# Kernel optimization log

Measured on AMD Instinct MI355X. Metric: run time of the kernel, lower is better.

The kernel has to match this reference:

```python
import jax, jax.numpy as jnp
import numpy as np

B, N, D = 512, 120, 64
NB = 8  # n_freq_bands
S_CLIP, DELTA_CLIP = 10.0, 5.0


def zc_rms(x, g, eps=1e-8):
    # zero-centred RMS norm
    x0 = x - x0_mean(x)
    return x0 * jax.lax.rsqrt(jnp.mean(x0 * x0, axis=-1, keepdims=True) + eps) * g


def x0_mean(x):
    return jnp.mean(x, axis=-1, keepdims=True)


def l2norm(x, eps=1e-8):
    return x * jax.lax.rsqrt(jnp.sum(x * x, axis=-1, keepdims=True) + eps)


def setup_inputs() -> dict:
    key = jax.random.key(0)
    ks = jax.random.split(key, 12)
    s = 1.0 / np.sqrt(D)
    return {
        "x": jax.random.normal(ks[0], (B, N, D), dtype=jnp.float32),
        "g_norm": jnp.ones((D,), jnp.float32),
        "Wq": jax.random.normal(ks[1], (D, D), jnp.float32) * s,
        "Wk": jax.random.normal(ks[2], (D, D), jnp.float32) * s,
        "Wv": jax.random.normal(ks[3], (D, D), jnp.float32) * s,
        "bv": jnp.zeros((D,), jnp.float32),
        "Wo": jax.random.normal(ks[4], (D, D), jnp.float32) * s,
        "bo": jnp.zeros((D,), jnp.float32),
        "g_post": jnp.ones((D,), jnp.float32),
        "W1": jax.random.normal(ks[5], (NB, 16), jnp.float32) * (1.0 / np.sqrt(NB)),
        "b1": jnp.zeros((16,), jnp.float32),
        "W2": jax.random.normal(ks[6], (16, 1), jnp.float32) * 0.25,
        "b2": jnp.full((1,), 0.5, jnp.float32),  # bias init 0.5 as in torch
    }


def _gamma(h, W1, b1, W2, b2):
    # FFT over embedding dim, band-averaged energies -> gate in [0.5, 0.99]
    fft = jnp.abs(jnp.fft.rfft(jax.lax.stop_gradient(h), axis=-1))  # (B,N,n_f)
    n_f = fft.shape[-1]
    bs = max(1, n_f // NB)
    bands = [fft[..., i * bs:min(i * bs + bs, n_f)].mean(-1) for i in range(NB)]
    energy = jnp.stack(bands, axis=-1)  # (B,N,NB)
    energy = energy / jnp.clip(jnp.sum(energy, axis=-1, keepdims=True), 1e-8)
    hdn = jax.nn.silu(energy @ W1 + b1)
    raw = jax.nn.sigmoid(hdn @ W2 + b2)  # (B,N,1)
    return 0.5 + 0.49 * raw


def reference(x, g_norm, Wq, Wk, Wv, bv, Wo, bo, g_post, W1, b1, W2, b2):
    h = zc_rms(x, g_norm)
    q = l2norm(h @ Wq)
    k = l2norm(h @ Wk)
    v = h @ Wv + bv
    gamma = _gamma(h, W1, b1, W2, b2)  # (B,N,1)

    # time-major for scan
    qT = jnp.moveaxis(q, 1, 0)      # (N,B,D)
    kT = jnp.moveaxis(k, 1, 0)
    vT = jnp.moveaxis(v, 1, 0)
    gT = jnp.moveaxis(gamma, 1, 0)  # (N,B,1)

    S0 = jnp.zeros((x.shape[0], D, D), x.dtype)

    def step(S, inp):
        q_t, k_t, v_t, g_t = inp
        pred = jnp.einsum('bde,be->bd', S, k_t)
        delta = jnp.clip(v_t - pred, -DELTA_CLIP, DELTA_CLIP)
        S = g_t[..., None] * S + delta[:, :, None] * k_t[:, None, :]
        S = jnp.clip(S, -S_CLIP, S_CLIP)
        o_t = jnp.einsum('bde,be->bd', S, q_t)
        return S, o_t

    _, outT = jax.lax.scan(step, S0, (qT, kT, vT, gT))
    out = jnp.moveaxis(outT, 0, 1)  # (B,N,D)
    out = zc_rms(out, g_post) @ Wo + bo  # dropout is identity at inference
    return x + out
```

## Files before the change

kernel.cpp:

```cpp
#include <hip/hip_runtime.h>
#include <math.h>

#define B_ 512
#define N_ 120

typedef __attribute__((ext_vector_type(8))) _Float16 f16x8;
typedef __attribute__((ext_vector_type(4))) _Float16 f16x4;
typedef __attribute__((ext_vector_type(2))) _Float16 f16x2;
typedef __attribute__((ext_vector_type(4))) float f32x4;
typedef __attribute__((ext_vector_type(2))) float f32x2;
typedef __attribute__((ext_vector_type(4))) int i32x4;

#define DPP_XOR1 0xB1
#define DPP_XOR2 0x4E
#define DPP_HMIR 0x141
#define DPP_MIR  0x140
template<int CTRL>
__device__ __forceinline__ float dpp_add(float v) {
    int x = __builtin_amdgcn_mov_dpp(__float_as_int(v), CTRL, 0xF, 0xF, true);
    return v + __int_as_float(x);
}

__device__ __forceinline__ float mix_lo(float a, int b, float c) {
    float d;
    asm("v_fma_mix_f32 %0, %1, %2, %3 op_sel:[0,0,0] op_sel_hi:[0,1,0]"
        : "=v"(d) : "v"(a), "v"(b), "v"(c));
    return d;
}
__device__ __forceinline__ float mix_hi(float a, int b, float c) {
    float d;
    asm("v_fma_mix_f32 %0, %1, %2, %3 op_sel:[0,1,0] op_sel_hi:[0,1,0]"
        : "=v"(d) : "v"(a), "v"(b), "v"(c));
    return d;
}
__device__ __forceinline__ f32x2 pk_mul2(f32x2 a, f32x2 b) {
    f32x2 d;
    asm("v_pk_mul_f32 %0, %1, %2" : "=v"(d) : "v"(a), "v"(b));
    return d;
}
__device__ __forceinline__ int pkrtz_i32(float a, float b) {
    auto sp = __builtin_amdgcn_cvt_pkrtz(a, b);
    return *(int*)&sp;
}

#define OFF_WQ 0
#define OFF_WK 4096
#define OFF_WV 8192
#define OFF_T  12288
#define OFF_XF 16384
#define OFF_QS 0
#define OFF_KS 7680
#define OFF_VS 15360
#define OFF_OF 23040
#define OFF_WO 31232
#define LDS_F16 35328

__device__ __forceinline__ void mm4(f16x8 a0, f16x8 a1, const _Float16* wmat,
                                    int lane, f32x4* acc) {
    const f16x8* wv = (const f16x8*)wmat;
    #pragma unroll
    for (int nt = 0; nt < 4; ++nt) {
        f32x4 z = {0.f, 0.f, 0.f, 0.f};
        z = __builtin_amdgcn_mfma_f32_16x16x32_f16(a0, wv[nt * 128 + lane], z, 0, 0, 0);
        z = __builtin_amdgcn_mfma_f32_16x16x32_f16(a1, wv[nt * 128 + 64 + lane], z, 0, 0, 0);
        acc[nt] = z;
    }
}

__global__ __launch_bounds__(512, 4) void fused_kdn(
    const float* __restrict__ x, const float* __restrict__ g_norm,
    const float* __restrict__ Wq, const float* __restrict__ Wk,
    const float* __restrict__ Wv, const float* __restrict__ bv,
    const float* __restrict__ Wo, const float* __restrict__ bo,
    const float* __restrict__ g_post,
    const float* __restrict__ W1, const float* __restrict__ b1,
    const float* __restrict__ W2, const float* __restrict__ b2,
    float* out)
{
    __shared__ __align__(16) _Float16 L[LDS_F16];
    __shared__ __align__(16) float g_s[N_];
    __shared__ float bv_s[64], bo_s[64];
    __shared__ float sW1[128], sb1[16], sW2[16], sb2_s[1];

    int tid = threadIdx.x, wave = tid >> 6, lane = tid & 63;
    int b = blockIdx.x;

    if (tid < 128) sW1[tid] = W1[tid];
    if (tid >= 128 && tid < 144) sb1[tid - 128] = b1[tid - 128];
    if (tid >= 144 && tid < 160) sW2[tid - 144] = W2[tid - 144];
    if (tid == 160) sb2_s[0] = b2[0];
    if (tid >= 192 && tid < 256) bv_s[tid - 192] = bv[tid - 192];
    if (tid >= 256 && tid < 320) bo_s[tid - 256] = bo[tid - 256];
    if (tid < 128) {
        f16x8 z = {0, 0, 0, 0, 0, 0, 0, 0};
        *(f16x8*)&L[OFF_XF + 7168 + tid * 8] = z;
        *(f16x8*)&L[OFF_OF + 7168 + tid * 8] = z;
    }
    int sn = tid & 63, sk0 = (tid >> 6) * 8;
    int widx = (sn >> 4) * 1024 + (sk0 >> 5) * 512 + ((((sk0 >> 3) & 3) << 4) + (sn & 15)) * 8;
    {
        const float* Ws[4] = { Wq, Wk, Wv, Wo };
        const int woff[4] = { OFF_WQ, OFF_WK, OFF_WV, OFF_WO };
        #pragma unroll
        for (int m = 0; m < 4; ++m) {
            f16x8 pv;
            #pragma unroll
            for (int j = 0; j < 8; ++j) pv[j] = (_Float16)Ws[m][(sk0 + j) * 64 + sn];
            *(f16x8*)&L[woff[m] + widx] = pv;
        }
        f16x8 pv;
        int nn = sn & 31;
        #pragma unroll
        for (int j = 0; j < 8; ++j) {
            int kk = ((sk0 + j) * nn) & 63;
            float a = (float)kk * (6.283185307179586f / 64.0f);
            float s, c; __sincosf(a, &s, &c);
            pv[j] = (_Float16)((sn < 32) ? c : s);
        }
        *(f16x8*)&L[OFF_T + widx] = pv;
    }
    __syncthreads();

    const float* xb = x + (size_t)b * N_ * 64;
    float* ob_g = out + (size_t)b * N_ * 64;

    {
        float gn = g_norm[lane];
        int hbase = (lane >> 5) * 512 + ((lane >> 3) & 3) * 128 + (lane & 7);
        #pragma unroll 5
        for (int c = 0; c < 15; ++c) {
            int row = wave * 15 + c;
            float xv = xb[row * 64 + lane];
            float sx = xv, sxx = xv * xv;
            sx = dpp_add<DPP_XOR1>(sx); sxx = dpp_add<DPP_XOR1>(sxx);
            sx = dpp_add<DPP_XOR2>(sx); sxx = dpp_add<DPP_XOR2>(sxx);
            sx = dpp_add<DPP_HMIR>(sx); sxx = dpp_add<DPP_HMIR>(sxx);
            sx = dpp_add<DPP_MIR >(sx); sxx = dpp_add<DPP_MIR >(sxx);
            sx += __shfl_xor(sx, 16);   sxx += __shfl_xor(sxx, 16);
            sx += __shfl_xor(sx, 32);   sxx += __shfl_xor(sxx, 32);
            float mean = sx * 0.015625f;
            float var  = sxx * 0.015625f - mean * mean;
            float h = (xv - mean) * rsqrtf(var + 1e-8f) * gn;
            float hp = __shfl_xor(h, 1);
            if (!(lane & 1)) {
                f16x2 pk2 = { (_Float16)h, (_Float16)hp };
                *(f16x2*)&L[OFF_XF + (row >> 4) * 1024 + (row & 15) * 8 + hbase] = pk2;
            }
        }
    }
    __syncthreads();

    int grp = lane >> 4, li = lane & 15;
    int rbase = wave * 16 + grp * 4;
    {
        const f16x8* hfv = (const f16x8*)(L + OFF_XF);
        f16x8 a0 = hfv[wave * 128 + lane];
        f16x8 a1 = hfv[wave * 128 + 64 + lane];
        f32x4 accT[4];

        mm4(a0, a1, L + OFF_T, lane, accT);
        {
            int gb2 = lane & 48;
            #pragma unroll
            for (int reg = 0; reg < 4; ++reg) {
                float re1 = accT[0][reg], re2 = accT[1][reg];
                float im1 = accT[2][reg], im2 = accT[3][reg];
                float m1 = sqrtf(fmaf(re1, re1, im1 * im1));
                float m2 = sqrtf(fmaf(re2, re2, im2 * im2));
                m1 = dpp_add<DPP_XOR1>(m1); m2 = dpp_add<DPP_XOR1>(m2);
                m1 = dpp_add<DPP_XOR2>(m1); m2 = dpp_add<DPP_XOR2>(m2);
                float e1 = m1 * 0.25f, e2 = m2 * 0.25f;
                float tot = e1 + e2;
                tot = dpp_add<DPP_HMIR>(tot);
                tot = dpp_add<DPP_MIR >(tot);
                float rinv = 1.0f / fmaxf(tot, 1e-8f);
                float en1 = e1 * rinv, en2 = e2 * rinv;
                float hs = sb1[li];
                #pragma unroll
                for (int i = 0; i < 4; ++i)
                    hs = fmaf(__shfl(en1, gb2 + (i << 2)), sW1[i * 16 + li], hs);
                #pragma unroll
                for (int i = 0; i < 4; ++i)
                    hs = fmaf(__shfl(en2, gb2 + (i << 2)), sW1[(i + 4) * 16 + li], hs);
                float act = hs / (1.0f + __expf(-hs));
                float p = act * sW2[li];
                p = dpp_add<DPP_XOR1>(p);
                p = dpp_add<DPP_XOR2>(p);
                p = dpp_add<DPP_HMIR>(p);
                p = dpp_add<DPP_MIR >(p);
                float raw = 1.0f / (1.0f + __expf(-(p + sb2_s[0])));
                int row = rbase + reg;
                if (li == 0 && row < N_) g_s[row] = fmaf(0.49f, raw, 0.5f);
            }
        }

        f32x4 accq[4], acck[4], accv[4];
        mm4(a0, a1, L + OFF_WQ, lane, accq);
        mm4(a0, a1, L + OFF_WK, lane, acck);
        mm4(a0, a1, L + OFF_WV, lane, accv);

        {
            f32x4 sq = accq[0]*accq[0] + accq[1]*accq[1] + accq[2]*accq[2] + accq[3]*accq[3];
            f32x4 sk = acck[0]*acck[0] + acck[1]*acck[1] + acck[2]*acck[2] + acck[3]*acck[3];
            #pragma unroll
            for (int reg = 0; reg < 4; ++reg) {
                float qs = sq[reg], ks = sk[reg];
                qs = dpp_add<DPP_XOR1>(qs); ks = dpp_add<DPP_XOR1>(ks);
                qs = dpp_add<DPP_XOR2>(qs); ks = dpp_add<DPP_XOR2>(ks);
                qs = dpp_add<DPP_HMIR>(qs); ks = dpp_add<DPP_HMIR>(ks);
                qs = dpp_add<DPP_MIR >(qs); ks = dpp_add<DPP_MIR >(ks);
                float rq = rsqrtf(qs + 1e-8f), rk = rsqrtf(ks + 1e-8f);
                #pragma unroll
                for (int nt = 0; nt < 4; ++nt) { accq[nt][reg] *= rq; acck[nt][reg] *= rk; }
            }
            #pragma unroll
            for (int nt = 0; nt < 4; ++nt) {
                float bvn = bv_s[nt * 16 + li];
                #pragma unroll
                for (int reg = 0; reg < 4; ++reg) accv[nt][reg] += bvn;
            }
        }
        __syncthreads();

        #pragma unroll
        for (int reg = 0; reg < 4; ++reg) {
            int row = rbase + reg;
            if (row < N_) {
                int base = row * 64 + li;
                #pragma unroll
                for (int nt = 0; nt < 4; ++nt) {
                    L[OFF_QS + base + nt * 16] = (_Float16)accq[nt][reg];
                    L[OFF_KS + base + nt * 16] = (_Float16)acck[nt][reg];
                    L[OFF_VS + base + nt * 16] = (_Float16)accv[nt][reg];
                }
            }
        }
    }
    __syncthreads();

    if (wave < 4) {
        int col = lane & 15;
        int kg  = lane >> 4;
        int c0  = kg * 8;
        int d0  = wave * 16 + kg * 4;
        int dpart = (d0 >> 5) * 512 + ((d0 >> 3) & 3) * 128 + (d0 & 7);
        const _Float16* ksp = L + OFF_KS;
        const _Float16* qsp = L + OFF_QS;
        const _Float16* vsp = L + OFF_VS;
        const _Float16* bbase = (col == 0) ? (qsp + c0) : (ksp + 64 + c0);
        const _Float16* vown = vsp + d0 + (col & 3);
        int srcli = (col & 3) ? (col & 3) : 4;
        int bp_addr = (((col >> 2) << 4) + srcli) << 2;

        f32x2 S2[8];
        #pragma unroll
        for (int j = 0; j < 8; ++j) { S2[j].x = 0.f; S2[j].y = 0.f; }
        f32x4 ppC = {0.f, 0.f, 0.f, 0.f};
        const float fone = 1.0f, fzero = 0.0f;
        float4 gq = *(const float4*)&g_s[0];

#define UPD2(j, KW, DST)                                                       \
        {                                                                      \
            f32x2 t2 = pk_mul2(gt2, S2[j]);                                    \
            float sa = mix_lo(delta, KW, t2.x);                                \
            float sb = mix_hi(delta, KW, t2.y);                                \
            sa = __builtin_amdgcn_fmed3f(sa, -10.f, 10.f);                     \
            sb = __builtin_amdgcn_fmed3f(sb, -10.f, 10.f);                     \
            S2[j].x = sa; S2[j].y = sb;                                        \
            DST = pkrtz_i32(sa, sb);                                           \
        }

#define SCAN_IT(T, GT)                                                         \
        {                                                                      \
            int   vv  = (int)*(const unsigned short*)&vown[(T) * 64];          \
            f16x8 ku0 = *(const f16x8*)&ksp[(T) * 64 + c0];                    \
            f16x8 ku1 = *(const f16x8*)&ksp[(T) * 64 + c0 + 32];               \
            f16x8 b0  = *(const f16x8*)&bbase[(T) * 64];                       \
            f16x8 b1  = *(const f16x8*)&bbase[(T) * 64 + 32];                  \
            float gt = (GT);                                                   \
            f32x2 gt2; gt2.x = gt; gt2.y = gt;                                 \
            float pA = (col & 1) ? ppC[1] : ppC[0];                            \
            float pB = (col & 1) ? ppC[3] : ppC[2];                            \
            float pown = (col & 2) ? pB : pA;                                  \
            float vf = mix_lo(fone, vv, fzero);                                \
            float dloc = __builtin_amdgcn_fmed3f(vf - pown, -5.f, 5.f);        \
            float delta = __int_as_float(                                      \
                __builtin_amdgcn_ds_bpermute(bp_addr, __float_as_int(dloc)));  \
            i32x4 k0i = *(i32x4*)&ku0;                                         \
            i32x4 k1i = *(i32x4*)&ku1;                                         \
            i32x4 a0i, a1i;                                                    \
            UPD2(0, k0i[0], a0i[0]) UPD2(1, k0i[1], a0i[1])                    \
            UPD2(2, k0i[2], a0i[2]) UPD2(3, k0i[3], a0i[3])                    \
            UPD2(4, k1i[0], a1i[0]) UPD2(5, k1i[1], a1i[1])                    \
            UPD2(6, k1i[2], a1i[2]) UPD2(7, k1i[3], a1i[3])                    \
            f16x8 a0s = *(f16x8*)&a0i;                                         \
            f16x8 a1s = *(f16x8*)&a1i;                                         \
            f32x4 C = {0.f, 0.f, 0.f, 0.f};                                    \
            C = __builtin_amdgcn_mfma_f32_16x16x32_f16(a0s, b0, C, 0, 0, 0);   \
            C = __builtin_amdgcn_mfma_f32_16x16x32_f16(a1s, b1, C, 0, 0, 0);   \
            if (col == 0) {                                                    \
                f16x4 o4 = { (_Float16)C[0], (_Float16)C[1],                   \
                             (_Float16)C[2], (_Float16)C[3] };                 \
                int oidx = OFF_OF + (((T) >> 4) * 1024) + (((T) & 15) * 8) + dpart; \
                *(f16x4*)&L[oidx] = o4;                                        \
            }                                                                  \
            ppC = C;                                                           \
        }

        for (int t4 = 0; t4 < N_; t4 += 4) {
            float4 gq_n = (t4 + 4 < N_) ? *(const float4*)&g_s[t4 + 4] : gq;
            SCAN_IT(t4 + 0, gq.x)
            SCAN_IT(t4 + 1, gq.y)
            SCAN_IT(t4 + 2, gq.z)
            SCAN_IT(t4 + 3, gq.w)
            gq = gq_n;
        }
#undef SCAN_IT
#undef UPD2
    }
    __syncthreads();

    {
        float gp = g_post[lane];
        int hbase = (lane >> 5) * 512 + ((lane >> 3) & 3) * 128 + (lane & 7);
        #pragma unroll 5
        for (int c = 0; c < 15; ++c) {
            int row = wave * 15 + c;
            int ridx = OFF_OF + (row >> 4) * 1024 + (row & 15) * 8;
            float ov = (float)L[ridx + hbase];
            float sx = ov, sxx = ov * ov;
            sx = dpp_add<DPP_XOR1>(sx); sxx = dpp_add<DPP_XOR1>(sxx);
            sx = dpp_add<DPP_XOR2>(sx); sxx = dpp_add<DPP_XOR2>(sxx);
            sx = dpp_add<DPP_HMIR>(sx); sxx = dpp_add<DPP_HMIR>(sxx);
            sx = dpp_add<DPP_MIR >(sx); sxx = dpp_add<DPP_MIR >(sxx);
            sx += __shfl_xor(sx, 16);   sxx += __shfl_xor(sxx, 16);
            sx += __shfl_xor(sx, 32);   sxx += __shfl_xor(sxx, 32);
            float mean = sx * 0.015625f;
            float var  = sxx * 0.015625f - mean * mean;
            float hn = (ov - mean) * rsqrtf(var + 1e-8f) * gp;
            float hp = __shfl_xor(hn, 1);
            if (!(lane & 1)) {
                f16x2 pk2 = { (_Float16)hn, (_Float16)hp };
                *(f16x2*)&L[ridx + hbase] = pk2;
            }
        }
    }
    __syncthreads();

    {
        const f16x8* hfv = (const f16x8*)(L + OFF_OF);
        f16x8 a0 = hfv[wave * 128 + lane];
        f16x8 a1 = hfv[wave * 128 + 64 + lane];
        f32x4 acc[4];
        mm4(a0, a1, L + OFF_WO, lane, acc);
        #pragma unroll
        for (int reg = 0; reg < 4; ++reg) {
            int row = rbase + reg;
            if (row < N_) {
                #pragma unroll
                for (int nt = 0; nt < 4; ++nt) {
                    int idx = row * 64 + nt * 16 + li;
                    ob_g[idx] = acc[nt][reg] + bo_s[nt * 16 + li] + xb[idx];
                }
            }
        }
    }
}

extern "C" void kernel_launch(void* const* d_in, const int* in_sizes, int n_in,
                              void* d_out, int out_size, void* d_ws, size_t ws_size,
                              hipStream_t stream)
{
    const float* x      = (const float*)d_in[0];
    const float* g_norm = (const float*)d_in[1];
    const float* Wq     = (const float*)d_in[2];
    const float* Wk     = (const float*)d_in[3];
    const float* Wv     = (const float*)d_in[4];
    const float* bv     = (const float*)d_in[5];
    const float* Wo     = (const float*)d_in[6];
    const float* bo     = (const float*)d_in[7];
    const float* g_post = (const float*)d_in[8];
    const float* W1     = (const float*)d_in[9];
    const float* b1     = (const float*)d_in[10];
    const float* W2     = (const float*)d_in[11];
    const float* b2     = (const float*)d_in[12];
    float* out = (float*)d_out;

    fused_kdn<<<B_, 512, 0, stream>>>(x, g_norm, Wq, Wk, Wv, bv, Wo, bo, g_post,
                                      W1, b1, W2, b2, out);
}
```

Measured before the change: 146.8 us.

## Restructure scan MFMA so state is B operand and delta computed without bpermute

The recurrence inner step now uses the updated state as the MFMA B operand, with q and the next k as A operands, in two separate MFMA pairs. The output and the next step's prediction land directly in the lane that owns each row. The v term is folded in as the accumulator init (-v), which removes the ds_bpermute cross-lane shuffle and the per-lane select of the previous C from the serial dependency chain. In exchange it issues four MFMAs per step instead of two, and the final iteration reads k and v one row past N, which may touch out-of-range shared memory.

```diff
diff --git a/kernel.cpp b/kernel.cpp
--- a/kernel.cpp
+++ b/kernel.cpp
@@ -242,21 +242,26 @@
         int col = lane & 15;
         int kg  = lane >> 4;
         int c0  = kg * 8;
-        int d0  = wave * 16 + kg * 4;
-        int dpart = (d0 >> 5) * 512 + ((d0 >> 3) & 3) * 128 + (d0 & 7);
-        const _Float16* ksp = L + OFF_KS;
-        const _Float16* qsp = L + OFF_QS;
-        const _Float16* vsp = L + OFF_VS;
-        const _Float16* bbase = (col == 0) ? (qsp + c0) : (ksp + 64 + c0);
-        const _Float16* vown = vsp + d0 + (col & 3);
-        int srcli = (col & 3) ? (col & 3) : 4;
-        int bp_addr = (((col >> 2) << 4) + srcli) << 2;
+        int dd  = wave * 16 + col;
+        int dpart = (dd >> 5) * 512 + ((dd >> 3) & 3) * 128 + (dd & 7);
+        const _Float16* ksp  = L + OFF_KS;
+        const _Float16* qsp  = L + OFF_QS;
+        const _Float16* vown = L + OFF_VS + dd;
 
         f32x2 S2[8];
         #pragma unroll
         for (int j = 0; j < 8; ++j) { S2[j].x = 0.f; S2[j].y = 0.f; }
-        f32x4 ppC = {0.f, 0.f, 0.f, 0.f};
-        const float fone = 1.0f, fzero = 0.0f;
+        const float fzero = 0.0f, fnegone = -1.0f;
+
+        f16x8 ku0 = *(const f16x8*)&ksp[c0];
+        f16x8 ku1 = *(const f16x8*)&ksp[c0 + 32];
+        float delta;
+        {
+            int vv0 = (int)*(const unsigned short*)&vown[0];
+            float mv = mix_lo(fnegone, vv0, fzero);
+            float dneg = __builtin_amdgcn_fmed3f(mv, -5.f, 5.f);
+            delta = __int_as_float(__float_as_int(dneg) ^ 0x80000000);
+        }
         float4 gq = *(const float4*)&g_s[0];
 
 #define UPD2(j, KW, DST)                                                       \
@@ -272,20 +277,13 @@
 
 #define SCAN_IT(T, GT)                                                         \
         {                                                                      \
-            int   vv  = (int)*(const unsigned short*)&vown[(T) * 64];          \
-            f16x8 ku0 = *(const f16x8*)&ksp[(T) * 64 + c0];                    \
-            f16x8 ku1 = *(const f16x8*)&ksp[(T) * 64 + c0 + 32];               \
-            f16x8 b0  = *(const f16x8*)&bbase[(T) * 64];                       \
-            f16x8 b1  = *(const f16x8*)&bbase[(T) * 64 + 32];                  \
+            f16x8 kn0 = *(const f16x8*)&ksp[((T) + 1) * 64 + c0];              \
+            f16x8 kn1 = *(const f16x8*)&ksp[((T) + 1) * 64 + c0 + 32];         \
+            f16x8 q0  = *(const f16x8*)&qsp[(T) * 64 + c0];                    \
+            f16x8 q1  = *(const f16x8*)&qsp[(T) * 64 + c0 + 32];               \
+            int   vv  = (int)*(const unsigned short*)&vown[((T) + 1) * 64];    \
             float gt = (GT);                                                   \
             f32x2 gt2; gt2.x = gt; gt2.y = gt;                                 \
-            float pA = (col & 1) ? ppC[1] : ppC[0];                            \
-            float pB = (col & 1) ? ppC[3] : ppC[2];                            \
-            float pown = (col & 2) ? pB : pA;                                  \
-            float vf = mix_lo(fone, vv, fzero);                                \
-            float dloc = __builtin_amdgcn_fmed3f(vf - pown, -5.f, 5.f);        \
-            float delta = __int_as_float(                                      \
-                __builtin_amdgcn_ds_bpermute(bp_addr, __float_as_int(dloc)));  \
             i32x4 k0i = *(i32x4*)&ku0;                                         \
             i32x4 k1i = *(i32x4*)&ku1;                                         \
             i32x4 a0i, a1i;                                                    \
@@ -295,16 +293,19 @@
             UPD2(6, k1i[2], a1i[2]) UPD2(7, k1i[3], a1i[3])                    \
             f16x8 a0s = *(f16x8*)&a0i;                                         \
             f16x8 a1s = *(f16x8*)&a1i;                                         \
-            f32x4 C = {0.f, 0.f, 0.f, 0.f};                                    \
-            C = __builtin_amdgcn_mfma_f32_16x16x32_f16(a0s, b0, C, 0, 0, 0);   \
-            C = __builtin_amdgcn_mfma_f32_16x16x32_f16(a1s, b1, C, 0, 0, 0);   \
-            if (col == 0) {                                                    \
-                f16x4 o4 = { (_Float16)C[0], (_Float16)C[1],                   \
-                             (_Float16)C[2], (_Float16)C[3] };                 \
-                int oidx = OFF_OF + (((T) >> 4) * 1024) + (((T) & 15) * 8) + dpart; \
-                *(f16x4*)&L[oidx] = o4;                                        \
-            }                                                                  \
-            ppC = C;                                                           \
+            f32x4 Co = {0.f, 0.f, 0.f, 0.f};                                   \
+            Co = __builtin_amdgcn_mfma_f32_16x16x32_f16(q0, a0s, Co, 0, 0, 0); \
+            Co = __builtin_amdgcn_mfma_f32_16x16x32_f16(q1, a1s, Co, 0, 0, 0); \
+            if (kg == 0)                                                       \
+                L[OFF_OF + (((T) >> 4) * 1024) + (((T) & 15) * 8) + dpart] =   \
+                    (_Float16)Co[0];                                           \
+            float mv = mix_lo(fnegone, vv, fzero);                             \
+            f32x4 Cd = {mv, mv, mv, mv};                                       \
+            Cd = __builtin_amdgcn_mfma_f32_16x16x32_f16(kn0, a0s, Cd, 0, 0, 0);\
+            Cd = __builtin_amdgcn_mfma_f32_16x16x32_f16(kn1, a1s, Cd, 0, 0, 0);\
+            float dneg = __builtin_amdgcn_fmed3f(Cd[0], -5.f, 5.f);            \
+            delta = __int_as_float(__float_as_int(dneg) ^ 0x80000000);         \
+            ku0 = kn0; ku1 = kn1;                                              \
         }
 
         for (int t4 = 0; t4 < N_; t4 += 4) {
```

After: 149.6 us. About the same (+1.9%).
